# Performance work log

Hardware: AMD Instinct MI355X
Metric: run time of the kernel (lower is better)

Reference implementation:

```python
import jax, jax.numpy as jnp
import numpy as np


def _ln(x, w, b, eps=1e-5):
    mu = x.mean(-1, keepdims=True)
    var = x.var(-1, keepdims=True)
    return (x - mu) / jnp.sqrt(var + eps) * w + b


def setup_inputs() -> dict:
    b, n, c, h, m = 2, 4096, 256, 8, 48
    T = (2 * (2048 // 4 - 1) + 1) ** 2  # 1023^2 = 1046529 rel-pos table rows
    hid = int(c * 2.0)  # mlp_ratio = 2.0
    ks = jax.random.split(jax.random.key(0), 24)
    std = 0.02
    inp = {
        'feat': jax.random.normal(ks[0], (b, n, c), jnp.float32),
        'cluster_mask': jnp.ones((b, n, m), jnp.float32),
        'pre_table': jax.random.normal(ks[1], (T, 5), jnp.float32),
        'norm1_w': jnp.ones((c,), jnp.float32),
        'norm1_b': jnp.zeros((c,), jnp.float32),
        'q_w': jax.random.normal(ks[2], (c, c), jnp.float32) * std,
        'q_b': jnp.zeros((c,), jnp.float32),
        'kv_w': jax.random.normal(ks[3], (2 * c, c), jnp.float32) * std,
        'kv_b': jnp.zeros((2 * c,), jnp.float32),
        'blank_k': jax.random.normal(ks[4], (c,), jnp.float32),
        'blank_v': jax.random.normal(ks[5], (c,), jnp.float32),
        'pe_w': jax.random.normal(ks[6], (h, 5), jnp.float32) * std,
        'pe_b': jnp.zeros((h,), jnp.float32),
        'proj_w': jax.random.normal(ks[7], (c, c), jnp.float32) * std,
        'proj_b': jnp.zeros((c,), jnp.float32),
        'norm2_w': jnp.ones((c,), jnp.float32),
        'norm2_b': jnp.zeros((c,), jnp.float32),
        'fc1_w': jax.random.normal(ks[8], (hid, c), jnp.float32) * std,
        'fc1_b': jnp.zeros((hid,), jnp.float32),
        'fc2_w': jax.random.normal(ks[9], (c, hid), jnp.float32) * std,
        'fc2_b': jnp.zeros((c,), jnp.float32),
        'member_idx': jax.random.randint(ks[10], (b, n, m), 0, n, jnp.int32),
        'pe_idx': jax.random.randint(ks[11], (b, n, m), 0, T, jnp.int32),
        'global_attn': 0,
    }
    return inp


def reference(feat, cluster_mask, pre_table, norm1_w, norm1_b, q_w, q_b, kv_w, kv_b,
              blank_k, blank_v, pe_w, pe_b, proj_w, proj_b, norm2_w, norm2_b,
              fc1_w, fc1_b, fc2_w, fc2_b, member_idx, pe_idx, global_attn):
    # ClusterTransformerBlock forward, local (global_attn=False) path.
    b, n, c = feat.shape
    h = pe_w.shape[0]
    c_ = c // h
    x = _ln(feat, norm1_w, norm1_b)
    q = (x @ q_w.T + q_b) * (c_ ** -0.5)            # b n c
    kv = (x @ kv_w.T + kv_b).reshape(b, n, h, 2, c_)
    key, v = kv[..., 0, :], kv[..., 1, :]           # b n h c_
    qh = q.reshape(b, n, h, c_)
    bi = jnp.arange(b)[:, None, None]
    k_nb = key[bi, member_idx]                      # b n m h c_ (CLUSTENQK gather)
    v_nb = v[bi, member_idx]                        # b n m h c_
    attn = jnp.einsum('bnhc,bnmhc->bhnm', qh, k_nb)
    pe_table = pre_table @ pe_w.T + pe_b            # T h
    pos = pe_table[pe_idx]                          # b n m h
    attn = attn + pos.transpose(0, 3, 1, 2)
    attn = attn + ((1.0 - cluster_mask) * -100.0)[:, None]
    blank = jnp.einsum('bnhc,hc->bhn', qh, blank_k.reshape(h, c_))[..., None]
    full = jax.nn.softmax(jnp.concatenate([attn, blank], axis=-1), axis=-1)
    attn_w, blank_w = full[..., :-1], full[..., -1]
    out = jnp.einsum('bhnm,bnmhc->bnhc', attn_w, v_nb)      # CLUSTENAV
    out = out + jnp.einsum('bhn,hc->bnhc', blank_w, blank_v.reshape(h, c_))
    out = out.reshape(b, n, c) @ proj_w.T + proj_b
    feat = feat + out
    y = _ln(feat, norm2_w, norm2_b)
    y = jax.nn.gelu(y @ fc1_w.T + fc1_b, approximate=False)
    y = y @ fc2_w.T + fc2_b
    return feat + y
```

## Files before the change

### kernel.cpp

```cpp
#include <hip/hip_runtime.h>
#include <hip/hip_bf16.h>
#include <hip/hip_fp8.h>
#include <cstdint>
#include <cstddef>

typedef __bf16 bf16;
typedef bf16 bf16x4 __attribute__((ext_vector_type(4)));
typedef bf16 bf16x8 __attribute__((ext_vector_type(8)));
typedef float f32x4 __attribute__((ext_vector_type(4)));
typedef float f32x2 __attribute__((ext_vector_type(2)));
typedef _Float16 h16;

__device__ __forceinline__ float fp8_to_f32(uint8_t b) {
  __hip_fp8_e4m3 t; t.__x = (__hip_fp8_storage_t)b; return (float)t;
}
__device__ __forceinline__ uint8_t f32_to_fp8(float v) {
  __hip_fp8_e4m3 t(v); return (uint8_t)t.__x;
}
__device__ __forceinline__ void cvt4_fp8(int w, float* f) {
#if __has_builtin(__builtin_amdgcn_cvt_pk_f32_fp8)
  f32x2 a = __builtin_amdgcn_cvt_pk_f32_fp8(w, false);
  f32x2 b = __builtin_amdgcn_cvt_pk_f32_fp8(w, true);
  f[0] = a[0]; f[1] = a[1]; f[2] = b[0]; f[3] = b[1];
#else
  f[0] = fp8_to_f32((uint8_t)w);
  f[1] = fp8_to_f32((uint8_t)(w >> 8));
  f[2] = fp8_to_f32((uint8_t)(w >> 16));
  f[3] = fp8_to_f32((uint8_t)(w >> 24));
#endif
}

__device__ __forceinline__ int kv_perm_to_orig(int j) {
  int jj = j & 255, h = jj >> 5, c = jj & 31;
  return h * 64 + ((j >> 8) ? 32 : 0) + c;
}

__global__ __launch_bounds__(256) void prep_posm_ln_kernel(
    const float* __restrict__ q_w, const float* __restrict__ kv_w,
    const float* __restrict__ proj_w, const float* __restrict__ fc1_w,
    const float* __restrict__ fc2_w, const float* __restrict__ q_b,
    const float* __restrict__ kv_b,
    bf16* __restrict__ wqkvs, bf16* __restrict__ wprojs,
    bf16* __restrict__ wfc1s, bf16* __restrict__ wfc2s,
    float* __restrict__ qscale, float* __restrict__ qbias,
    const int* __restrict__ pe_idx,
    const float* __restrict__ cluster_mask,
    const float* __restrict__ pre_table,
    const float* __restrict__ pe_w, const float* __restrict__ pe_b,
    h16* __restrict__ posm,
    const float* __restrict__ feat,
    const float* __restrict__ norm1_w, const float* __restrict__ norm1_b,
    bf16* __restrict__ xbuf)
{
  const int b = blockIdx.x;
  if (b < 768) {
    int i = b * 256 + threadIdx.x;
    if (i < 196608) {
      int e = i & 7, r16 = (i >> 3) & 15, part = (i >> 7) & 3,
          c = (i >> 9) & 31, panel = i >> 14;
      int fn = c >> 3, p2 = c & 7;
      int ncol = panel * 64 + fn * 16 + r16;
      int k = p2 * 32 + part * 8 + e;
      float v;
      if (ncol < 256) v = q_w[(size_t)ncol * 256 + k];
      else            v = kv_w[(size_t)kv_perm_to_orig(ncol - 256) * 256 + k];
      wqkvs[i] = (bf16)v;
    }
    if (i < 65536) {
      int e = i & 7, r16 = (i >> 3) & 15, part = (i >> 7) & 3,
          c = (i >> 9) & 15, panel = i >> 13;
      int fn = c >> 3, p2 = c & 7;
      int ncol = panel * 32 + fn * 16 + r16;
      int k = p2 * 32 + part * 8 + e;
      wprojs[i] = (bf16)proj_w[(size_t)ncol * 256 + k];
    }
    if (i < 131072) {
      {
        int e = i & 7, r16 = (i >> 3) & 15, part = (i >> 7) & 3,
            p2 = (i >> 9) & 7, fn = i >> 12;
        wfc1s[i] = (bf16)fc1_w[(size_t)(fn * 16 + r16) * 256 + p2 * 32 + part * 8 + e];
      }
      {
        int e = i & 7, r16 = (i >> 3) & 15, part = (i >> 7) & 3,
            p2 = (i >> 9) & 15, fn = i >> 13;
        wfc2s[i] = (bf16)fc2_w[(size_t)(fn * 16 + r16) * 512 + p2 * 32 + part * 8 + e];
      }
    }
    if (i < 768) {
      const float s = 0.17677669529663687f;
      if (i < 256) { qscale[i] = s;    qbias[i] = q_b[i] * s; }
      else         { qscale[i] = 1.0f; qbias[i] = kv_b[kv_perm_to_orig(i - 256)]; }
    }
  } else if (b < 2304) {
    int i = (b - 768) * 256 + threadIdx.x;
    int pj = pe_idx[i];
    const float* pt = pre_table + (size_t)pj * 5;
    float p0 = pt[0], p1 = pt[1], p2 = pt[2], p3 = pt[3], p4 = pt[4];
    float mk = (1.0f - cluster_mask[i]) * -100.0f;
    h16 v8[8];
    #pragma unroll
    for (int h = 0; h < 8; ++h) {
      float v = p0 * pe_w[h*5+0] + p1 * pe_w[h*5+1] + p2 * pe_w[h*5+2]
              + p3 * pe_w[h*5+3] + p4 * pe_w[h*5+4] + pe_b[h] + mk;
      v8[h] = (h16)v;
    }
    *((uint4*)(posm + (size_t)i * 8)) = *(const uint4*)v8;
  } else {
    const int wv = threadIdx.x >> 6, lane = threadIdx.x & 63;
    const int row = (b - 2304) * 4 + wv;
    f32x4 v = *((const f32x4*)(feat + (size_t)row * 256) + lane);
    float s  = v[0] + v[1] + v[2] + v[3];
    float s2 = v[0]*v[0] + v[1]*v[1] + v[2]*v[2] + v[3]*v[3];
    #pragma unroll
    for (int o = 1; o < 64; o <<= 1) { s += __shfl_xor(s, o); s2 += __shfl_xor(s2, o); }
    float mu = s * (1.0f / 256.0f);
    float var = s2 * (1.0f / 256.0f) - mu * mu;
    float rstd = rsqrtf(var + 1e-5f);
    f32x4 wv4 = *((const f32x4*)norm1_w + lane);
    f32x4 bv4 = *((const f32x4*)norm1_b + lane);
    bf16x4 o4;
    o4[0] = (bf16)((v[0] - mu) * rstd * wv4[0] + bv4[0]);
    o4[1] = (bf16)((v[1] - mu) * rstd * wv4[1] + bv4[1]);
    o4[2] = (bf16)((v[2] - mu) * rstd * wv4[2] + bv4[2]);
    o4[3] = (bf16)((v[3] - mu) * rstd * wv4[3] + bv4[3]);
    *((bf16x4*)(xbuf + (size_t)row * 256) + lane) = o4;
  }
}

template<int NF, int K>
__global__ __launch_bounds__(256) void gemm_bt(
    const bf16* __restrict__ A, const bf16* __restrict__ Bf,
    int N,
    const float* __restrict__ scale, const float* __restrict__ bias,
    const float* __restrict__ residualf, const bf16* __restrict__ residualh,
    int do_gelu,
    float* __restrict__ outf, bf16* __restrict__ outh,
    bf16* __restrict__ outq, uint8_t* __restrict__ outkv)
{
  constexpr int KP = K / 32;
  constexpr int NCH = NF * KP;
  __shared__ __align__(16) bf16 ldsB[NCH * 512];
  const int tid = threadIdx.x;
  const int w = tid >> 6, lane = tid & 63;
  const int part = lane >> 4, r16 = lane & 15;
  const int rowBase = blockIdx.x * 128 + w * 32;
  const int colBase = blockIdx.y * (NF * 16);
  const bf16* Bpanel = Bf + (size_t)blockIdx.y * NCH * 512;

  for (int c = w; c < NCH; c += 4) {
    __builtin_amdgcn_global_load_lds(
        (const __attribute__((address_space(1))) uint32_t*)(Bpanel + c * 512 + lane * 8),
        (__attribute__((address_space(3))) uint32_t*)&ldsB[c * 512], 16, 0, 0);
  }

  f32x4 acc[2][NF] = {};
  const bf16* Aw0 = A + (size_t)(rowBase + r16) * K + part * 8;
  const bf16* Aw1 = A + (size_t)(rowBase + 16 + r16) * K + part * 8;
  __syncthreads();

  #pragma unroll
  for (int p2 = 0; p2 < KP; ++p2) {
    bf16x8 af0 = *(const bf16x8*)(Aw0 + p2 * 32);
    bf16x8 af1 = *(const bf16x8*)(Aw1 + p2 * 32);
    bf16x8 bfr[NF];
    #pragma unroll
    for (int fn = 0; fn < NF; ++fn)
      bfr[fn] = *(const bf16x8*)&ldsB[(fn * KP + p2) * 512 + lane * 8];
    #pragma unroll
    for (int fn = 0; fn < NF; ++fn) {
      acc[0][fn] = __builtin_amdgcn_mfma_f32_16x16x32_bf16(af0, bfr[fn], acc[0][fn], 0, 0, 0);
      acc[1][fn] = __builtin_amdgcn_mfma_f32_16x16x32_bf16(af1, bfr[fn], acc[1][fn], 0, 0, 0);
    }
  }

  #pragma unroll
  for (int fm = 0; fm < 2; ++fm)
  #pragma unroll
  for (int fn = 0; fn < NF; ++fn)
  #pragma unroll
  for (int r = 0; r < 4; ++r) {
    int row = rowBase + fm * 16 + part * 4 + r;
    int col = colBase + fn * 16 + r16;
    float v = acc[fm][fn][r];
    if (scale)     v *= scale[col];
    if (bias)      v += bias[col];
    if (do_gelu)   v = 0.5f * v * (1.0f + erff(v * 0.70710678118654752f));
    if (residualf) v += residualf[(size_t)row * N + col];
    if (residualh) v += (float)residualh[(size_t)row * N + col];
    if (outq) {
      if (col < 256) outq[(size_t)row * 256 + col] = (bf16)v;
      else           outkv[(size_t)row * 512 + (col - 256)] = f32_to_fp8(v);
    } else if (outf) {
      outf[(size_t)row * N + col] = v;
    } else {
      outh[(size_t)row * N + col] = (bf16)v;
    }
  }
}

__global__ __launch_bounds__(512) void mlp_ln_kernel(
    const bf16* __restrict__ trunk,
    const float* __restrict__ lnw, const float* __restrict__ lnb,
    const bf16* __restrict__ W1s,
    const float* __restrict__ b1,
    const bf16* __restrict__ W2s,
    const float* __restrict__ b2,
    float* __restrict__ out)
{
  __shared__ __align__(16) bf16 xr[16][264];
  __shared__ __align__(16) bf16 y1[16][520];
  const int tid = threadIdx.x;
  const int w = tid >> 6, lane = tid & 63;
  const int part = lane >> 4, r16 = lane & 15;
  const int rowBase = blockIdx.x * 16;

  #pragma unroll
  for (int rr = 0; rr < 2; ++rr) {
    const int r = w * 2 + rr;
    bf16x4 vh = *((const bf16x4*)(trunk + (size_t)(rowBase + r) * 256) + lane);
    float v0 = (float)vh[0], v1 = (float)vh[1], v2 = (float)vh[2], v3 = (float)vh[3];
    float s  = v0 + v1 + v2 + v3;
    float s2 = v0*v0 + v1*v1 + v2*v2 + v3*v3;
    #pragma unroll
    for (int o = 1; o < 64; o <<= 1) { s += __shfl_xor(s, o); s2 += __shfl_xor(s2, o); }
    float mu = s * (1.0f / 256.0f);
    float var = s2 * (1.0f / 256.0f) - mu * mu;
    float rstd = rsqrtf(var + 1e-5f);
    f32x4 wv4 = *((const f32x4*)lnw + lane);
    f32x4 bv4 = *((const f32x4*)lnb + lane);
    bf16x4 o4;
    o4[0] = (bf16)((v0 - mu) * rstd * wv4[0] + bv4[0]);
    o4[1] = (bf16)((v1 - mu) * rstd * wv4[1] + bv4[1]);
    o4[2] = (bf16)((v2 - mu) * rstd * wv4[2] + bv4[2]);
    o4[3] = (bf16)((v3 - mu) * rstd * wv4[3] + bv4[3]);
    *((bf16x4*)&xr[r][lane * 4]) = o4;
  }
  __syncthreads();

  {
    f32x4 acc[4] = {};
    #pragma unroll
    for (int p2 = 0; p2 < 8; ++p2) {
      bf16x8 af = *(const bf16x8*)&xr[r16][p2 * 32 + part * 8];
      #pragma unroll
      for (int fn = 0; fn < 4; ++fn) {
        const int gfn = w * 4 + fn;
        bf16x8 bf_ = *(const bf16x8*)(W1s + ((size_t)((gfn * 8 + p2) * 4 + part) * 16 + r16) * 8);
        acc[fn] = __builtin_amdgcn_mfma_f32_16x16x32_bf16(af, bf_, acc[fn], 0, 0, 0);
      }
    }
    #pragma unroll
    for (int fn = 0; fn < 4; ++fn)
    #pragma unroll
    for (int r = 0; r < 4; ++r) {
      int row = part * 4 + r;
      int col = w * 64 + fn * 16 + r16;
      float v = acc[fn][r] + b1[col];
      v = 0.5f * v * (1.0f + erff(v * 0.70710678118654752f));
      y1[row][col] = (bf16)v;
    }
  }
  __syncthreads();

  {
    f32x4 acc[2] = {};
    #pragma unroll
    for (int p2 = 0; p2 < 16; ++p2) {
      bf16x8 af = *(const bf16x8*)&y1[r16][p2 * 32 + part * 8];
      #pragma unroll
      for (int fn = 0; fn < 2; ++fn) {
        const int gfn = w * 2 + fn;
        bf16x8 bf_ = *(const bf16x8*)(W2s + ((size_t)((gfn * 16 + p2) * 4 + part) * 16 + r16) * 8);
        acc[fn] = __builtin_amdgcn_mfma_f32_16x16x32_bf16(af, bf_, acc[fn], 0, 0, 0);
      }
    }
    #pragma unroll
    for (int fn = 0; fn < 2; ++fn)
    #pragma unroll
    for (int r = 0; r < 4; ++r) {
      int row = rowBase + part * 4 + r;
      int col = w * 32 + fn * 16 + r16;
      float v = acc[fn][r] + b2[col] + (float)trunk[(size_t)row * 256 + col];
      out[(size_t)row * 256 + col] = v;
    }
  }
}

__global__ __launch_bounds__(256) void attn_kernel(
    const bf16* __restrict__ qb,
    const uint8_t* __restrict__ kvf8,
    const int* __restrict__ member_idx,
    const h16* __restrict__ posm,
    const float* __restrict__ blank_k, const float* __restrict__ blank_v,
    bf16* __restrict__ out)
{
  const int wv = threadIdx.x >> 6, lane = threadIdx.x & 63;
  const int bid = blockIdx.x;
  const int xcd = bid & 7, grp = bid >> 3;
  const int token = (xcd >> 2) * 4096 + (xcd & 3) * 1024 + grp * 4 + wv;
  const int bb = token >> 12;
  const int n = lane >> 4;
  const int hc = lane & 15;
  const int h = hc >> 1, cb = hc & 1;
  const int ch0 = h * 32 + cb * 16;

  float q[16];
  {
    const bf16* qrow = qb + (size_t)token * 256 + ch0;
    #pragma unroll
    for (int c8 = 0; c8 < 2; ++c8) {
      bf16x8 t = *(const bf16x8*)(qrow + c8 * 8);
      #pragma unroll
      for (int e = 0; e < 8; ++e) q[c8 * 8 + e] = (float)t[e];
    }
  }

  int   midx[12];
  float pos[12];
  #pragma unroll
  for (int m = 0; m < 12; ++m) {
    midx[m] = member_idx[(size_t)token * 48 + m * 4 + n];
    pos[m]  = (float)posm[(size_t)token * 384 + (m * 4 + n) * 8 + h];
  }

  float l = 0.0f, o[16] = {};
  {
    float db = 0.0f;
    #pragma unroll
    for (int c = 0; c < 16; ++c) db += q[c] * blank_k[ch0 + c];
    db += __shfl_xor(db, 1);
    float pb = __expf(db);
    if (n == 0) {
      l = pb;
      #pragma unroll
      for (int c = 0; c < 16; ++c) o[c] = pb * blank_v[ch0 + c];
    }
  }

  const uint8_t* kvb = kvf8 + (size_t)(bb * 4096) * 512;
  #pragma unroll
  for (int m = 0; m < 12; ++m) {
    const uint8_t* kp = kvb + (size_t)midx[m] * 512 + ch0;
    int4 kw = *(const int4*)kp;
    int4 vw = *(const int4*)(kp + 256);

    float kf[4];
    float d = 0.0f;
    cvt4_fp8(kw.x, kf);
    #pragma unroll
    for (int c = 0; c < 4; ++c) d += q[c] * kf[c];
    cvt4_fp8(kw.y, kf);
    #pragma unroll
    for (int c = 0; c < 4; ++c) d += q[4 + c] * kf[c];
    cvt4_fp8(kw.z, kf);
    #pragma unroll
    for (int c = 0; c < 4; ++c) d += q[8 + c] * kf[c];
    cvt4_fp8(kw.w, kf);
    #pragma unroll
    for (int c = 0; c < 4; ++c) d += q[12 + c] * kf[c];

    d += __shfl_xor(d, 1);
    float p = __expf(d + pos[m]);
    l += p;

    float vf[4];
    cvt4_fp8(vw.x, vf);
    #pragma unroll
    for (int c = 0; c < 4; ++c) o[c] += p * vf[c];
    cvt4_fp8(vw.y, vf);
    #pragma unroll
    for (int c = 0; c < 4; ++c) o[4 + c] += p * vf[c];
    cvt4_fp8(vw.z, vf);
    #pragma unroll
    for (int c = 0; c < 4; ++c) o[8 + c] += p * vf[c];
    cvt4_fp8(vw.w, vf);
    #pragma unroll
    for (int c = 0; c < 4; ++c) o[12 + c] += p * vf[c];
  }

  l += __shfl_xor(l, 16); l += __shfl_xor(l, 32);
  #pragma unroll
  for (int c = 0; c < 16; ++c) {
    o[c] += __shfl_xor(o[c], 16);
    o[c] += __shfl_xor(o[c], 32);
  }

  if (n == 0) {
    float inv = 1.0f / l;
    bf16* orow = out + (size_t)token * 256 + ch0;
    #pragma unroll
    for (int c8 = 0; c8 < 2; ++c8) {
      bf16x8 t;
      #pragma unroll
      for (int e = 0; e < 8; ++e) t[e] = (bf16)(o[c8 * 8 + e] * inv);
      *(bf16x8*)(orow + c8 * 8) = t;
    }
  }
}

extern "C" void kernel_launch(void* const* d_in, const int* in_sizes, int n_in,
                              void* d_out, int out_size, void* d_ws, size_t ws_size,
                              hipStream_t stream)
{
  (void)in_sizes; (void)n_in; (void)out_size; (void)ws_size;
  const float* feat         = (const float*)d_in[0];
  const float* cluster_mask = (const float*)d_in[1];
  const float* pre_table    = (const float*)d_in[2];
  const float* norm1_w      = (const float*)d_in[3];
  const float* norm1_b      = (const float*)d_in[4];
  const float* q_w    = (const float*)d_in[5];
  const float* q_b    = (const float*)d_in[6];
  const float* kv_w   = (const float*)d_in[7];
  const float* kv_b   = (const float*)d_in[8];
  const float* blank_k = (const float*)d_in[9];
  const float* blank_v = (const float*)d_in[10];
  const float* pe_w   = (const float*)d_in[11];
  const float* pe_b   = (const float*)d_in[12];
  const float* proj_w = (const float*)d_in[13];
  const float* proj_b = (const float*)d_in[14];
  const float* norm2_w = (const float*)d_in[15];
  const float* norm2_b = (const float*)d_in[16];
  const float* fc1_w  = (const float*)d_in[17];
  const float* fc1_b  = (const float*)d_in[18];
  const float* fc2_w  = (const float*)d_in[19];
  const float* fc2_b  = (const float*)d_in[20];
  const int* member_idx = (const int*)d_in[21];
  const int* pe_idx     = (const int*)d_in[22];

  char* ws = (char*)d_ws;
  size_t off = 0;
  auto alloc = [&](size_t bytes) -> void* {
    void* p = ws + off; off += (bytes + 255) & ~(size_t)255; return p;
  };
  bf16*  wqkvs = (bf16*)alloc(768 * 256 * sizeof(bf16));
  bf16*  wprojs = (bf16*)alloc(256 * 256 * sizeof(bf16));
  bf16*  wfc1s = (bf16*)alloc(512 * 256 * sizeof(bf16));
  bf16*  wfc2s = (bf16*)alloc(256 * 512 * sizeof(bf16));
  float* qscale = (float*)alloc(768 * sizeof(float));
  float* qbias  = (float*)alloc(768 * sizeof(float));
  bf16*    xbuf   = (bf16*)alloc((size_t)8192 * 256 * sizeof(bf16));
  bf16*    qb     = (bf16*)alloc((size_t)8192 * 256 * sizeof(bf16));
  uint8_t* kvf8   = (uint8_t*)alloc((size_t)8192 * 512);
  bf16*    attnb  = (bf16*)alloc((size_t)8192 * 256 * sizeof(bf16));
  bf16*    feat2h = (bf16*)alloc((size_t)8192 * 256 * sizeof(bf16));
  h16*     posm   = (h16*)alloc((size_t)8192 * 48 * 8 * sizeof(h16));
  float* outf = (float*)d_out;

  prep_posm_ln_kernel<<<dim3(4352), dim3(256), 0, stream>>>(
      q_w, kv_w, proj_w, fc1_w, fc2_w, q_b, kv_b,
      wqkvs, wprojs, wfc1s, wfc2s, qscale, qbias,
      pe_idx, cluster_mask, pre_table, pe_w, pe_b, posm,
      feat, norm1_w, norm1_b, xbuf);
  gemm_bt<4, 256><<<dim3(64, 12), dim3(256), 0, stream>>>(
      xbuf, wqkvs, 768, qscale, qbias,
      (const float*)nullptr, (const bf16*)nullptr, 0,
      (float*)nullptr, (bf16*)nullptr, qb, kvf8);
  attn_kernel<<<dim3(2048), dim3(256), 0, stream>>>(
      qb, kvf8, member_idx, posm, blank_k, blank_v, attnb);
  gemm_bt<2, 256><<<dim3(64, 8), dim3(256), 0, stream>>>(
      attnb, wprojs, 256, (const float*)nullptr, proj_b,
      feat, (const bf16*)nullptr, 0,
      (float*)nullptr, feat2h, (bf16*)nullptr, (uint8_t*)nullptr);
  mlp_ln_kernel<<<dim3(512), dim3(512), 0, stream>>>(
      feat2h, norm2_w, norm2_b, wfc1s, fc1_b, wfc2s, fc2_b, outf);
}
```

Measured before the change: 84.64 us.

## Fuse output projection and residual add into attention kernel

The attention kernel now processes 16 tokens per 1024-thread block, stages each token's attention output in shared memory, and then runs the output projection with MFMA, adding bias and the residual before writing feat2h directly. This removes the separate projection GEMM launch and the round trip of the attention buffer through global memory. In exchange, blocks are much larger (1024 threads), which may reduce occupancy and scheduling flexibility, and the projection weights are reread from global memory by every block.

Result: slower. 95.71 us (+13.1%).

```diff
diff --git a/kernel.cpp b/kernel.cpp
--- a/kernel.cpp
+++ b/kernel.cpp
@@ -286,18 +286,25 @@
   }
 }
 
-__global__ __launch_bounds__(256) void attn_kernel(
+__global__ __launch_bounds__(1024) void attn_proj_kernel(
     const bf16* __restrict__ qb,
     const uint8_t* __restrict__ kvf8,
     const int* __restrict__ member_idx,
     const h16* __restrict__ posm,
     const float* __restrict__ blank_k, const float* __restrict__ blank_v,
-    bf16* __restrict__ out)
+    const bf16* __restrict__ Wp,
+    const float* __restrict__ pbias,
+    const float* __restrict__ resid,
+    bf16* __restrict__ feat2h)
 {
-  const int wv = threadIdx.x >> 6, lane = threadIdx.x & 63;
+  __shared__ __align__(16) bf16 ao[16][264];
+  const int tid = threadIdx.x;
+  const int w = tid >> 6, lane = tid & 63;
+  const int part = lane >> 4, r16 = lane & 15;
   const int bid = blockIdx.x;
   const int xcd = bid & 7, grp = bid >> 3;
-  const int token = (xcd >> 2) * 4096 + (xcd & 3) * 1024 + grp * 4 + wv;
+  const int tokBase = (xcd >> 2) * 4096 + (xcd & 3) * 1024 + grp * 16;
+  const int token = tokBase + w;
   const int bb = token >> 12;
   const int n = lane >> 4;
   const int hc = lane & 15;
@@ -387,13 +394,32 @@
 
   if (n == 0) {
     float inv = 1.0f / l;
-    bf16* orow = out + (size_t)token * 256 + ch0;
     #pragma unroll
     for (int c8 = 0; c8 < 2; ++c8) {
       bf16x8 t;
       #pragma unroll
       for (int e = 0; e < 8; ++e) t[e] = (bf16)(o[c8 * 8 + e] * inv);
-      *(bf16x8*)(orow + c8 * 8) = t;
+      *(bf16x8*)&ao[w][ch0 + c8 * 8] = t;
+    }
+  }
+  __syncthreads();
+
+  {
+    f32x4 acc = {};
+    const int panel = w >> 1, fn = w & 1;
+    const bf16* Wbase = Wp + (size_t)panel * 8192 + (size_t)(fn * 8) * 512;
+    #pragma unroll
+    for (int p2 = 0; p2 < 8; ++p2) {
+      bf16x8 af = *(const bf16x8*)&ao[r16][p2 * 32 + part * 8];
+      bf16x8 bf_ = *(const bf16x8*)(Wbase + p2 * 512 + lane * 8);
+      acc = __builtin_amdgcn_mfma_f32_16x16x32_bf16(af, bf_, acc, 0, 0, 0);
+    }
+    #pragma unroll
+    for (int r = 0; r < 4; ++r) {
+      int row = tokBase + part * 4 + r;
+      int col = w * 16 + r16;
+      float v = acc[r] + pbias[col] + resid[(size_t)row * 256 + col];
+      feat2h[(size_t)row * 256 + col] = (bf16)v;
     }
   }
 }
@@ -441,7 +467,6 @@
   bf16*    xbuf   = (bf16*)alloc((size_t)8192 * 256 * sizeof(bf16));
   bf16*    qb     = (bf16*)alloc((size_t)8192 * 256 * sizeof(bf16));
   uint8_t* kvf8   = (uint8_t*)alloc((size_t)8192 * 512);
-  bf16*    attnb  = (bf16*)alloc((size_t)8192 * 256 * sizeof(bf16));
   bf16*    feat2h = (bf16*)alloc((size_t)8192 * 256 * sizeof(bf16));
   h16*     posm   = (h16*)alloc((size_t)8192 * 48 * 8 * sizeof(h16));
   float* outf = (float*)d_out;
@@ -455,12 +480,9 @@
       xbuf, wqkvs, 768, qscale, qbias,
       (const float*)nullptr, (const bf16*)nullptr, 0,
       (float*)nullptr, (bf16*)nullptr, qb, kvf8);
-  attn_kernel<<<dim3(2048), dim3(256), 0, stream>>>(
-      qb, kvf8, member_idx, posm, blank_k, blank_v, attnb);
-  gemm_bt<2, 256><<<dim3(64, 8), dim3(256), 0, stream>>>(
-      attnb, wprojs, 256, (const float*)nullptr, proj_b,
-      feat, (const bf16*)nullptr, 0,
-      (float*)nullptr, feat2h, (bf16*)nullptr, (uint8_t*)nullptr);
+  attn_proj_kernel<<<dim3(512), dim3(1024), 0, stream>>>(
+      qb, kvf8, member_idx, posm, blank_k, blank_v,
+      wprojs, proj_b, feat, feat2h);
   mlp_ln_kernel<<<dim3(512), dim3(512), 0, stream>>>(
       feat2h, norm2_w, norm2_b, wfc1s, fc1_b, wfc2s, fc2_b, outf);
 }
```
